# Optimization experiments

Measured on AMD Instinct MI355X. Metric: run time of the kernel, lower is better.

## Reference

```python
import jax, jax.numpy as jnp
import numpy as np

N, STATE_DIM, HID, D_EMB, K = 8192, 512, 128, 128, 10
EPS = 0.001


def setup_inputs() -> dict:
    key = jax.random.key(0)
    ks = jax.random.split(key, 5)
    sc = lambda fan_in: 1.0 / np.sqrt(fan_in)
    return {
        "s": jax.random.normal(ks[0], (N, STATE_DIM), dtype=jnp.float32),
        "W1": jax.random.normal(ks[1], (HID, STATE_DIM), dtype=jnp.float32) * sc(STATE_DIM),
        "b1": jax.random.normal(ks[2], (HID,), dtype=jnp.float32) * sc(STATE_DIM),
        "W2": jax.random.normal(ks[3], (D_EMB, HID), dtype=jnp.float32) * sc(HID),
        "b2": jax.random.normal(ks[4], (D_EMB,), dtype=jnp.float32) * sc(HID),
        "k": K,
    }


def reference(s, W1, b1, W2, b2, k):
    # embedding: relu(Linear) -> Linear
    x = jax.nn.relu(s @ W1.T + b1) @ W2.T + b2            # [N, d_emb]
    # pairwise L2 distance matrix: ||xi||^2 + ||xj||^2 - 2 xi.xj
    sq = jnp.sum(x * x, axis=1)                            # [N]
    dist2 = sq[:, None] + sq[None, :] - 2.0 * (x @ x.T)    # [N, N]
    # clamp tiny negative values from cancellation (torch.sqrt would NaN)
    dist = jnp.sqrt(jnp.maximum(dist2, 1e-12))             # [N, N]
    # k nearest per row, excluding self (smallest entry = own distance ~0)
    neg_vals, _ = jax.lax.top_k(-dist, k + 1)              # [N, k+1], ascending dist
    k_nearest = -neg_vals[:, 1:]                           # [N, k]
    sum_k_nearest = jnp.sum(k_nearest, axis=1, keepdims=True)  # [N, 1]
    mean_k_nearest_2 = jnp.mean(sum_k_nearest) ** 2
    return EPS / (sum_k_nearest ** 2 / mean_k_nearest_2 + EPS)
```

## Files before the change

### kernel.cpp

```cpp
#include <hip/hip_runtime.h>
#include <hip/hip_bf16.h>

#define NN 8192
#define SD 512
#define HID 128
#define DE 128
#define KP1 11
#define EPSF 0.001f
#define NSPLIT 16
#define NCHUNK NSPLIT
#define TILE 64
#define NTILE ((NN / NSPLIT) / TILE)

using short8 = __attribute__((ext_vector_type(8))) short;
using f32x4 = __attribute__((ext_vector_type(4))) float;

__device__ inline ushort f2bf(float f) {
    __hip_bfloat16 b = __float2bfloat16(f);
    return *reinterpret_cast<ushort*>(&b);
}
__device__ inline float bf2f(ushort u) {
    unsigned v = (unsigned)u << 16;
    union { unsigned u; float f; } c; c.u = v; return c.f;
}

__global__ __launch_bounds__(256) void wsplit_kernel(
    const float* __restrict__ W1, const float* __restrict__ W2,
    ushort* __restrict__ W1h, ushort* __restrict__ W1l,
    ushort* __restrict__ W2h, ushort* __restrict__ W2l)
{
    const int bid = blockIdx.x;
    const float* src; ushort *dh, *dl; int base;
    if (bid < 64) { src = W1; dh = W1h; dl = W1l; base = bid * 1024; }
    else          { src = W2; dh = W2h; dl = W2l; base = (bid - 64) * 1024; }
    const int i = base + threadIdx.x * 4;
    float4 f = *reinterpret_cast<const float4*>(src + i);
    ushort h[4], lo[4];
    float fv[4] = {f.x, f.y, f.z, f.w};
#pragma unroll
    for (int j = 0; j < 4; ++j) {
        h[j] = f2bf(fv[j]);
        lo[j] = f2bf(fv[j] - bf2f(h[j]));
    }
    *reinterpret_cast<uint2*>(dh + i) = *reinterpret_cast<uint2*>(h);
    *reinterpret_cast<uint2*>(dl + i) = *reinterpret_cast<uint2*>(lo);
}

__global__ __launch_bounds__(256) void mlp_kernel(
    const float* __restrict__ s, const ushort* __restrict__ W1h,
    const ushort* __restrict__ W1l, const float* __restrict__ b1,
    const ushort* __restrict__ W2h, const ushort* __restrict__ W2l,
    const float* __restrict__ b2, __hip_bfloat16* __restrict__ xb,
    float* __restrict__ sqb)
{
    __shared__ __align__(16) ushort sbh[2][32 * 32];
    __shared__ __align__(16) ushort sbl[2][32 * 32];
    __shared__ __align__(16) ushort hbh[32 * 128];
    __shared__ __align__(16) ushort hbl[32 * 128];
    __shared__ __align__(16) ushort xtile[32 * 128];
    __shared__ float sqpart[4 * 32];

    const int t = threadIdx.x;
    const int w = t >> 6, l = t & 63;
    const int lc = l & 15, c4 = l >> 4;
    const int rb = blockIdx.x * 32;
    const int cb = w * 32;

    const int srow = t >> 3, skq = t & 7;
    const int ssl = ((skq >> 1) + (srow >> 2)) & 3;
    const int sByte = srow * 64 + (ssl ^ (srow & 3)) * 16 + (skq & 1) * 8;
    const float* sgbase = s + (size_t)(rb + srow) * SD + skq * 4;

    float4 sf;
#define STAGE_LOAD_S(kt_) sf = *reinterpret_cast<const float4*>(sgbase + (kt_) * 32)
#define STAGE_WRITE_S(b_) do { \
    float fv_[4] = {sf.x, sf.y, sf.z, sf.w}; \
    ushort h_[4], lo_[4]; \
    _Pragma("unroll") \
    for (int j_ = 0; j_ < 4; ++j_) { \
        h_[j_] = f2bf(fv_[j_]); \
        lo_[j_] = f2bf(fv_[j_] - bf2f(h_[j_])); \
    } \
    *reinterpret_cast<uint2*>(reinterpret_cast<char*>(sbh[b_]) + sByte) = *reinterpret_cast<uint2*>(h_); \
    *reinterpret_cast<uint2*>(reinterpret_cast<char*>(sbl[b_]) + sByte) = *reinterpret_cast<uint2*>(lo_); \
} while (0)

    int aByte[2];
#pragma unroll
    for (int rt = 0; rt < 2; ++rt) {
        int row = rt * 16 + lc;
        int sl = ((c4 + (row >> 2)) & 3) ^ (row & 3);
        aByte[rt] = row * 64 + sl * 16;
    }

    const ushort* w1hp[2]; const ushort* w1lp[2];
#pragma unroll
    for (int ct = 0; ct < 2; ++ct) {
        int col = cb + ct * 16 + lc;
        w1hp[ct] = W1h + (size_t)col * SD + c4 * 8;
        w1lp[ct] = W1l + (size_t)col * SD + c4 * 8;
    }

    f32x4 acc1[2][2];
#pragma unroll
    for (int rt = 0; rt < 2; ++rt)
#pragma unroll
        for (int ct = 0; ct < 2; ++ct) acc1[rt][ct] = {0.f, 0.f, 0.f, 0.f};

    STAGE_LOAD_S(0);
    STAGE_WRITE_S(0);
    short8 bh[2], bl[2], nbh[2], nbl[2];
#pragma unroll
    for (int ct = 0; ct < 2; ++ct) {
        bh[ct] = *reinterpret_cast<const short8*>(w1hp[ct]);
        bl[ct] = *reinterpret_cast<const short8*>(w1lp[ct]);
    }

    for (int kt = 0; kt < 16; ++kt) {
        __syncthreads();
        if (kt < 15) STAGE_LOAD_S(kt + 1);
        short8 ah[2], al[2];
#pragma unroll
        for (int rt = 0; rt < 2; ++rt) {
            ah[rt] = *reinterpret_cast<const short8*>(
                reinterpret_cast<char*>(sbh[kt & 1]) + aByte[rt]);
            al[rt] = *reinterpret_cast<const short8*>(
                reinterpret_cast<char*>(sbl[kt & 1]) + aByte[rt]);
        }
        if (kt < 15) {
#pragma unroll
            for (int ct = 0; ct < 2; ++ct) {
                nbh[ct] = *reinterpret_cast<const short8*>(w1hp[ct] + (kt + 1) * 32);
                nbl[ct] = *reinterpret_cast<const short8*>(w1lp[ct] + (kt + 1) * 32);
            }
        }
#pragma unroll
        for (int rt = 0; rt < 2; ++rt)
#pragma unroll
            for (int ct = 0; ct < 2; ++ct) {
                acc1[rt][ct] = __builtin_amdgcn_mfma_f32_16x16x32_bf16(ah[rt], bh[ct], acc1[rt][ct], 0, 0, 0);
                acc1[rt][ct] = __builtin_amdgcn_mfma_f32_16x16x32_bf16(ah[rt], bl[ct], acc1[rt][ct], 0, 0, 0);
                acc1[rt][ct] = __builtin_amdgcn_mfma_f32_16x16x32_bf16(al[rt], bh[ct], acc1[rt][ct], 0, 0, 0);
            }
        if (kt < 15) {
            STAGE_WRITE_S((kt + 1) & 1);
#pragma unroll
            for (int ct = 0; ct < 2; ++ct) { bh[ct] = nbh[ct]; bl[ct] = nbl[ct]; }
        }
    }

    float b1v[2];
#pragma unroll
    for (int ct = 0; ct < 2; ++ct) b1v[ct] = b1[cb + ct * 16 + lc];
#pragma unroll
    for (int rt = 0; rt < 2; ++rt)
#pragma unroll
        for (int ct = 0; ct < 2; ++ct)
#pragma unroll
            for (int reg = 0; reg < 4; ++reg) {
                float v = fmaxf(acc1[rt][ct][reg] + b1v[ct], 0.f);
                ushort hh = f2bf(v);
                ushort hl = f2bf(v - bf2f(hh));
                int row = rt * 16 + c4 * 4 + reg;
                int kcol = cb + ct * 16 + lc;
                int sl = (kcol >> 3) ^ (row & 15);
                int byte = row * 256 + sl * 16 + (kcol & 7) * 2;
                *reinterpret_cast<ushort*>(reinterpret_cast<char*>(hbh) + byte) = hh;
                *reinterpret_cast<ushort*>(reinterpret_cast<char*>(hbl) + byte) = hl;
            }
    __syncthreads();

    f32x4 acc2[2][2];
#pragma unroll
    for (int rt = 0; rt < 2; ++rt)
#pragma unroll
        for (int ct = 0; ct < 2; ++ct) acc2[rt][ct] = {0.f, 0.f, 0.f, 0.f};

#pragma unroll
    for (int kt = 0; kt < 4; ++kt) {
        short8 ah[2], al[2];
#pragma unroll
        for (int rt = 0; rt < 2; ++rt) {
            int row = rt * 16 + lc;
            int sl = (kt * 4 + c4) ^ (row & 15);
            int byte = row * 256 + sl * 16;
            ah[rt] = *reinterpret_cast<const short8*>(reinterpret_cast<char*>(hbh) + byte);
            al[rt] = *reinterpret_cast<const short8*>(reinterpret_cast<char*>(hbl) + byte);
        }
        short8 wh[2], wl[2];
#pragma unroll
        for (int ct = 0; ct < 2; ++ct) {
            int col = cb + ct * 16 + lc;
            wh[ct] = *reinterpret_cast<const short8*>(W2h + (size_t)col * HID + kt * 32 + c4 * 8);
            wl[ct] = *reinterpret_cast<const short8*>(W2l + (size_t)col * HID + kt * 32 + c4 * 8);
        }
#pragma unroll
        for (int rt = 0; rt < 2; ++rt)
#pragma unroll
            for (int ct = 0; ct < 2; ++ct) {
                acc2[rt][ct] = __builtin_amdgcn_mfma_f32_16x16x32_bf16(ah[rt], wh[ct], acc2[rt][ct], 0, 0, 0);
                acc2[rt][ct] = __builtin_amdgcn_mfma_f32_16x16x32_bf16(ah[rt], wl[ct], acc2[rt][ct], 0, 0, 0);
                acc2[rt][ct] = __builtin_amdgcn_mfma_f32_16x16x32_bf16(al[rt], wh[ct], acc2[rt][ct], 0, 0, 0);
            }
    }

    float b2v[2];
#pragma unroll
    for (int ct = 0; ct < 2; ++ct) b2v[ct] = b2[cb + ct * 16 + lc];
    float p[8];
#pragma unroll
    for (int j = 0; j < 8; ++j) p[j] = 0.f;
#pragma unroll
    for (int rt = 0; rt < 2; ++rt)
#pragma unroll
        for (int ct = 0; ct < 2; ++ct)
#pragma unroll
            for (int reg = 0; reg < 4; ++reg) {
                float v = acc2[rt][ct][reg] + b2v[ct];
                ushort xv = f2bf(v);
                float xf = bf2f(xv);
                p[rt * 4 + reg] = fmaf(xf, xf, p[rt * 4 + reg]);
                int row = rt * 16 + c4 * 4 + reg;
                int e = cb + ct * 16 + lc;
                xtile[row * 128 + e] = xv;
            }
#pragma unroll
    for (int j = 0; j < 8; ++j) {
#pragma unroll
        for (int off = 8; off >= 1; off >>= 1) p[j] += __shfl_xor(p[j], off, 16);
    }
    if (lc == 0) {
#pragma unroll
        for (int rt = 0; rt < 2; ++rt)
#pragma unroll
            for (int reg = 0; reg < 4; ++reg)
                sqpart[w * 32 + rt * 16 + c4 * 4 + reg] = p[rt * 4 + reg];
    }
    __syncthreads();
    if (t < 32)
        sqb[rb + t] = sqpart[t] + sqpart[32 + t] + sqpart[64 + t] + sqpart[96 + t];
    const short8* xsv = reinterpret_cast<const short8*>(xtile);
    short8* xg = reinterpret_cast<short8*>(reinterpret_cast<ushort*>(xb) + (size_t)rb * DE);
    xg[t] = xsv[t];
    xg[t + 256] = xsv[t + 256];
}

__global__ __launch_bounds__(256) void knn_kernel(
    const ushort* __restrict__ xs, const float* __restrict__ sqb,
    float* __restrict__ part)
{
    __shared__ __align__(16) ushort lbuf[2][TILE * DE];
    __shared__ __align__(16) float sqs[NN / NSPLIT];

    const int bid = blockIdx.x;
    const int rid = bid >> 4, cid = bid & 15;
    const int t = threadIdx.x;
    const int w = t >> 6, l = t & 63;
    const int q16 = l & 15, lg = l >> 4;
    const int kk = lg * 8;
    const int qb = rid * 128 + w * 32;
    const int cstart = cid * (NN / NSPLIT);

    short8 bq[2][4];
#pragma unroll
    for (int qs = 0; qs < 2; ++qs)
#pragma unroll
        for (int kb = 0; kb < 4; ++kb)
            bq[qs][kb] = *reinterpret_cast<const short8*>(
                xs + (size_t)(qb + qs * 16 + q16) * DE + kb * 32 + kk);

    float m[2][KP1];
#pragma unroll
    for (int qs = 0; qs < 2; ++qs)
#pragma unroll
        for (int j = 0; j < KP1; ++j) m[qs][j] = 1e30f;

#define INS(qs_, v_) do { \
    float d2_ = (v_); \
    _Pragma("unroll") \
    for (int j_ = KP1 - 1; j_ >= 1; --j_) \
        m[qs_][j_] = __builtin_amdgcn_fmed3f(d2_, m[qs_][j_ - 1], m[qs_][j_]); \
    m[qs_][0] = fminf(d2_, m[qs_][0]); \
} while (0)

    if (t < 128)
        reinterpret_cast<float4*>(sqs)[t] =
            reinterpret_cast<const float4*>(sqb + cstart)[t];

    int gIdx[4], dIdx[4];
#pragma unroll
    for (int i = 0; i < 4; ++i) {
        int sl = t + 256 * i;
        int row = sl >> 4, col = sl & 15;
        gIdx[i] = row * DE + col * 8;
        dIdx[i] = (row * 16 + (col ^ (row & 7))) * 8;
    }
    int aIdx[4];
#pragma unroll
    for (int kb = 0; kb < 4; ++kb)
        aIdx[kb] = (q16 * 16 + ((kb * 4 + lg) ^ (q16 & 7))) * 8;

    short8 st[4];
#define STAGE_LOAD(tt_) do { \
    const ushort* sb_ = xs + (size_t)(cstart + (tt_) * TILE) * DE; \
    _Pragma("unroll") \
    for (int i_ = 0; i_ < 4; ++i_) \
        st[i_] = *reinterpret_cast<const short8*>(sb_ + gIdx[i_]); \
} while (0)
#define STAGE_WRITE(nb_) do { \
    _Pragma("unroll") \
    for (int i_ = 0; i_ < 4; ++i_) \
        *reinterpret_cast<short8*>(&lbuf[nb_][dIdx[i_]]) = st[i_]; \
} while (0)

    STAGE_LOAD(0);
    STAGE_WRITE(0);

    for (int tt = 0; tt < NTILE; ++tt) {
        __syncthreads();
        if (tt + 1 < NTILE) STAGE_LOAD(tt + 1);
        const ushort* lb = lbuf[tt & 1];
#pragma unroll
        for (int cs = 0; cs < 4; ++cs) {
            short8 fa[4];
#pragma unroll
            for (int kb = 0; kb < 4; ++kb)
                fa[kb] = *reinterpret_cast<const short8*>(lb + cs * 2048 + aIdx[kb]);
            float4 sv = *reinterpret_cast<const float4*>(sqs + tt * TILE + cs * 16 + lg * 4);
#pragma unroll
            for (int qs = 0; qs < 2; ++qs) {
                f32x4 acc = {0.f, 0.f, 0.f, 0.f};
#pragma unroll
                for (int kb = 0; kb < 4; ++kb)
                    acc = __builtin_amdgcn_mfma_f32_16x16x32_bf16(fa[kb], bq[qs][kb], acc, 0, 0, 0);
                INS(qs, fmaf(-2.f, acc[0], sv.x));
                INS(qs, fmaf(-2.f, acc[1], sv.y));
                INS(qs, fmaf(-2.f, acc[2], sv.z));
                INS(qs, fmaf(-2.f, acc[3], sv.w));
            }
        }
        if (tt + 1 < NTILE) STAGE_WRITE((tt + 1) & 1);
    }
#undef STAGE_LOAD
#undef STAGE_WRITE
#undef INS

    __syncthreads();
    float* mb = reinterpret_cast<float*>(lbuf);
#pragma unroll
    for (int qs = 0; qs < 2; ++qs)
#pragma unroll
        for (int j = 0; j < KP1; ++j)
            mb[(((w * 2 + qs) * 4 + lg) * KP1 + j) * 16 + q16] = m[qs][j];
    __syncthreads();
    if (l < 32) {
        const int qs = l >> 4, qq = l & 15;
        float mm[KP1];
#pragma unroll
        for (int j = 0; j < KP1; ++j)
            mm[j] = mb[(((w * 2 + qs) * 4 + 0) * KP1 + j) * 16 + qq];
#pragma unroll
        for (int g = 1; g < 4; ++g)
#pragma unroll
            for (int j = 0; j < KP1; ++j) {
                float d2 = mb[(((w * 2 + qs) * 4 + g) * KP1 + j) * 16 + qq];
#pragma unroll
                for (int jj = KP1 - 1; jj >= 1; --jj)
                    mm[jj] = __builtin_amdgcn_fmed3f(d2, mm[jj - 1], mm[jj]);
                mm[0] = fminf(d2, mm[0]);
            }
        const int q = qb + qs * 16 + qq;
#pragma unroll
        for (int j = 0; j < KP1; ++j)
            part[(size_t)(cid * KP1 + j) * NN + q] = mm[j];
    }
}

__global__ __launch_bounds__(256) void merge_kernel(
    const float* __restrict__ part, const float* __restrict__ sqb,
    float* __restrict__ sumk, float* __restrict__ psum)
{
    const int row = blockIdx.x * 256 + threadIdx.x;
    float m[KP1];
#pragma unroll
    for (int j = 0; j < KP1; ++j) m[j] = 1e30f;
#pragma unroll
    for (int ch = 0; ch < NCHUNK; ++ch) {
#pragma unroll
        for (int j = 0; j < KP1; ++j) {
            float d2 = part[(size_t)(ch * KP1 + j) * NN + row];
#pragma unroll
            for (int jj = KP1 - 1; jj >= 1; --jj)
                m[jj] = __builtin_amdgcn_fmed3f(d2, m[jj - 1], m[jj]);
            m[0] = fminf(d2, m[0]);
        }
    }
    const float sqq = sqb[row];
    float sum = 0.f;
#pragma unroll
    for (int j = 1; j < KP1; ++j)
        sum += sqrtf(fmaxf(m[j] + sqq, 1e-12f));
    sumk[row] = sum;

    float p = sum;
#pragma unroll
    for (int off = 32; off >= 1; off >>= 1) p += __shfl_xor(p, off, 64);
    __shared__ float red[4];
    if ((threadIdx.x & 63) == 0) red[threadIdx.x >> 6] = p;
    __syncthreads();
    if (threadIdx.x == 0) psum[blockIdx.x] = red[0] + red[1] + red[2] + red[3];
}

__global__ void reduce_kernel(const float* __restrict__ psum, float* __restrict__ qv)
{
    const int t = threadIdx.x;
    float p = (t < 32) ? psum[t] : 0.f;
#pragma unroll
    for (int off = 32; off >= 1; off >>= 1) p += __shfl_xor(p, off, 64);
    if (t == 0) {
        float mean = p * (1.0f / NN);
        qv[0] = EPSF * mean * mean;
    }
}

__global__ __launch_bounds__(256) void final_kernel(
    const float* __restrict__ sumk, const float* __restrict__ qv,
    float* __restrict__ out)
{
    const int i = blockIdx.x * 256 + threadIdx.x;
    const float qq = qv[0];
    const float sv = sumk[i];
    out[i] = qq / (fmaf(sv, sv, qq));
}

extern "C" void kernel_launch(void* const* d_in, const int* in_sizes, int n_in,
                              void* d_out, int out_size, void* d_ws, size_t ws_size,
                              hipStream_t stream)
{
    const float* s  = (const float*)d_in[0];
    const float* W1 = (const float*)d_in[1];
    const float* b1 = (const float*)d_in[2];
    const float* W2 = (const float*)d_in[3];
    const float* b2 = (const float*)d_in[4];
    float* out = (float*)d_out;

    char* ws = (char*)d_ws;
    __hip_bfloat16* xb = (__hip_bfloat16*)ws;
    float* sqb  = (float*)(ws + (size_t)NN * DE * 2);
    float* part = sqb + NN;
    float* sumk = part + (size_t)NCHUNK * KP1 * NN;
    float* psum = sumk + NN;
    float* qv   = psum + 32;
    ushort* W1h = (ushort*)(qv + 1);
    ushort* W1l = W1h + (size_t)HID * SD;
    ushort* W2h = W1l + (size_t)HID * SD;
    ushort* W2l = W2h + (size_t)DE * HID;

    wsplit_kernel<<<80, 256, 0, stream>>>(W1, W2, W1h, W1l, W2h, W2l);
    mlp_kernel<<<NN / 32, 256, 0, stream>>>(s, W1h, W1l, b1, W2h, W2l, b2, xb, sqb);
    knn_kernel<<<(NN / 128) * NSPLIT, 256, 0, stream>>>((const ushort*)xb, sqb, part);
    merge_kernel<<<NN / 256, 256, 0, stream>>>(part, sqb, sumk, psum);
    reduce_kernel<<<1, 64, 0, stream>>>(psum, qv);
    final_kernel<<<NN / 256, 256, 0, stream>>>(sumk, qv, out);
}
```

Measured before the change: 79.53 us.

## Pre-scale candidates by -2, fold norms into MFMA accumulator, double KNN column splits

The MLP kernel now also writes a bf16 copy of the embeddings scaled by -2. The KNN kernel streams that copy as candidates and seeds the MFMA accumulator with the squared norms, which removes the per-element fma before insertion. Column splits double to 32 with 32-row tiles, launch bounds request 6 waves per SIMD, and the final per-block merge is done one query half at a time to cut LDS use. This adds parallelism and occupancy but doubles the partial-results traffic seen by the merge kernel, adds an extra embedding write, and rounds -2x to bf16.

```diff
diff --git a/kernel.cpp b/kernel.cpp
--- a/kernel.cpp
+++ b/kernel.cpp
@@ -7,9 +7,9 @@
 #define DE 128
 #define KP1 11
 #define EPSF 0.001f
-#define NSPLIT 16
+#define NSPLIT 32
 #define NCHUNK NSPLIT
-#define TILE 64
+#define TILE 32
 #define NTILE ((NN / NSPLIT) / TILE)
 
 using short8 = __attribute__((ext_vector_type(8))) short;
@@ -51,13 +51,14 @@
     const ushort* __restrict__ W1l, const float* __restrict__ b1,
     const ushort* __restrict__ W2h, const ushort* __restrict__ W2l,
     const float* __restrict__ b2, __hip_bfloat16* __restrict__ xb,
-    float* __restrict__ sqb)
+    __hip_bfloat16* __restrict__ xb2, float* __restrict__ sqb)
 {
     __shared__ __align__(16) ushort sbh[2][32 * 32];
     __shared__ __align__(16) ushort sbl[2][32 * 32];
     __shared__ __align__(16) ushort hbh[32 * 128];
     __shared__ __align__(16) ushort hbl[32 * 128];
     __shared__ __align__(16) ushort xtile[32 * 128];
+    __shared__ __align__(16) ushort xtile2[32 * 128];
     __shared__ float sqpart[4 * 32];
 
     const int t = threadIdx.x;
@@ -223,6 +224,7 @@
                 int row = rt * 16 + c4 * 4 + reg;
                 int e = cb + ct * 16 + lc;
                 xtile[row * 128 + e] = xv;
+                xtile2[row * 128 + e] = f2bf(-2.f * xf);
             }
 #pragma unroll
     for (int j = 0; j < 8; ++j) {
@@ -243,17 +245,21 @@
     short8* xg = reinterpret_cast<short8*>(reinterpret_cast<ushort*>(xb) + (size_t)rb * DE);
     xg[t] = xsv[t];
     xg[t + 256] = xsv[t + 256];
-}
-
-__global__ __launch_bounds__(256) void knn_kernel(
-    const ushort* __restrict__ xs, const float* __restrict__ sqb,
-    float* __restrict__ part)
+    const short8* xsv2 = reinterpret_cast<const short8*>(xtile2);
+    short8* xg2 = reinterpret_cast<short8*>(reinterpret_cast<ushort*>(xb2) + (size_t)rb * DE);
+    xg2[t] = xsv2[t];
+    xg2[t + 256] = xsv2[t + 256];
+}
+
+__global__ __launch_bounds__(256, 6) void knn_kernel(
+    const ushort* __restrict__ xs, const ushort* __restrict__ xs2,
+    const float* __restrict__ sqb, float* __restrict__ part)
 {
     __shared__ __align__(16) ushort lbuf[2][TILE * DE];
     __shared__ __align__(16) float sqs[NN / NSPLIT];
 
     const int bid = blockIdx.x;
-    const int rid = bid >> 4, cid = bid & 15;
+    const int rid = bid >> 5, cid = bid & 31;
     const int t = threadIdx.x;
     const int w = t >> 6, l = t & 63;
     const int q16 = l & 15, lg = l >> 4;
@@ -283,13 +289,13 @@
     m[qs_][0] = fminf(d2_, m[qs_][0]); \
 } while (0)
 
-    if (t < 128)
+    if (t < 64)
         reinterpret_cast<float4*>(sqs)[t] =
             reinterpret_cast<const float4*>(sqb + cstart)[t];
 
-    int gIdx[4], dIdx[4];
-#pragma unroll
-    for (int i = 0; i < 4; ++i) {
+    int gIdx[2], dIdx[2];
+#pragma unroll
+    for (int i = 0; i < 2; ++i) {
         int sl = t + 256 * i;
         int row = sl >> 4, col = sl & 15;
         gIdx[i] = row * DE + col * 8;
@@ -300,17 +306,15 @@
     for (int kb = 0; kb < 4; ++kb)
         aIdx[kb] = (q16 * 16 + ((kb * 4 + lg) ^ (q16 & 7))) * 8;
 
-    short8 st[4];
+    short8 st[2];
 #define STAGE_LOAD(tt_) do { \
-    const ushort* sb_ = xs + (size_t)(cstart + (tt_) * TILE) * DE; \
-    _Pragma("unroll") \
-    for (int i_ = 0; i_ < 4; ++i_) \
-        st[i_] = *reinterpret_cast<const short8*>(sb_ + gIdx[i_]); \
+    const ushort* sb_ = xs2 + (size_t)(cstart + (tt_) * TILE) * DE; \
+    st[0] = *reinterpret_cast<const short8*>(sb_ + gIdx[0]); \
+    st[1] = *reinterpret_cast<const short8*>(sb_ + gIdx[1]); \
 } while (0)
 #define STAGE_WRITE(nb_) do { \
-    _Pragma("unroll") \
-    for (int i_ = 0; i_ < 4; ++i_) \
-        *reinterpret_cast<short8*>(&lbuf[nb_][dIdx[i_]]) = st[i_]; \
+    *reinterpret_cast<short8*>(&lbuf[nb_][dIdx[0]]) = st[0]; \
+    *reinterpret_cast<short8*>(&lbuf[nb_][dIdx[1]]) = st[1]; \
 } while (0)
 
     STAGE_LOAD(0);
@@ -321,7 +325,7 @@
         if (tt + 1 < NTILE) STAGE_LOAD(tt + 1);
         const ushort* lb = lbuf[tt & 1];
 #pragma unroll
-        for (int cs = 0; cs < 4; ++cs) {
+        for (int cs = 0; cs < 2; ++cs) {
             short8 fa[4];
 #pragma unroll
             for (int kb = 0; kb < 4; ++kb)
@@ -329,14 +333,14 @@
             float4 sv = *reinterpret_cast<const float4*>(sqs + tt * TILE + cs * 16 + lg * 4);
 #pragma unroll
             for (int qs = 0; qs < 2; ++qs) {
-                f32x4 acc = {0.f, 0.f, 0.f, 0.f};
+                f32x4 acc = {sv.x, sv.y, sv.z, sv.w};
 #pragma unroll
                 for (int kb = 0; kb < 4; ++kb)
                     acc = __builtin_amdgcn_mfma_f32_16x16x32_bf16(fa[kb], bq[qs][kb], acc, 0, 0, 0);
-                INS(qs, fmaf(-2.f, acc[0], sv.x));
-                INS(qs, fmaf(-2.f, acc[1], sv.y));
-                INS(qs, fmaf(-2.f, acc[2], sv.z));
-                INS(qs, fmaf(-2.f, acc[3], sv.w));
+                INS(qs, acc[0]);
+                INS(qs, acc[1]);
+                INS(qs, acc[2]);
+                INS(qs, acc[3]);
             }
         }
         if (tt + 1 < NTILE) STAGE_WRITE((tt + 1) & 1);
@@ -345,34 +349,34 @@
 #undef STAGE_WRITE
 #undef INS
 
-    __syncthreads();
     float* mb = reinterpret_cast<float*>(lbuf);
 #pragma unroll
-    for (int qs = 0; qs < 2; ++qs)
+    for (int qs = 0; qs < 2; ++qs) {
+        __syncthreads();
 #pragma unroll
         for (int j = 0; j < KP1; ++j)
-            mb[(((w * 2 + qs) * 4 + lg) * KP1 + j) * 16 + q16] = m[qs][j];
-    __syncthreads();
-    if (l < 32) {
-        const int qs = l >> 4, qq = l & 15;
-        float mm[KP1];
-#pragma unroll
-        for (int j = 0; j < KP1; ++j)
-            mm[j] = mb[(((w * 2 + qs) * 4 + 0) * KP1 + j) * 16 + qq];
-#pragma unroll
-        for (int g = 1; g < 4; ++g)
-#pragma unroll
-            for (int j = 0; j < KP1; ++j) {
-                float d2 = mb[(((w * 2 + qs) * 4 + g) * KP1 + j) * 16 + qq];
-#pragma unroll
-                for (int jj = KP1 - 1; jj >= 1; --jj)
-                    mm[jj] = __builtin_amdgcn_fmed3f(d2, mm[jj - 1], mm[jj]);
-                mm[0] = fminf(d2, mm[0]);
-            }
-        const int q = qb + qs * 16 + qq;
-#pragma unroll
-        for (int j = 0; j < KP1; ++j)
-            part[(size_t)(cid * KP1 + j) * NN + q] = mm[j];
+            mb[((w * 4 + lg) * KP1 + j) * 16 + q16] = m[qs][j];
+        __syncthreads();
+        if (l < 16) {
+            float mm[KP1];
+#pragma unroll
+            for (int j = 0; j < KP1; ++j)
+                mm[j] = mb[((w * 4 + 0) * KP1 + j) * 16 + l];
+#pragma unroll
+            for (int g = 1; g < 4; ++g)
+#pragma unroll
+                for (int j = 0; j < KP1; ++j) {
+                    float d2 = mb[((w * 4 + g) * KP1 + j) * 16 + l];
+#pragma unroll
+                    for (int jj = KP1 - 1; jj >= 1; --jj)
+                        mm[jj] = __builtin_amdgcn_fmed3f(d2, mm[jj - 1], mm[jj]);
+                    mm[0] = fminf(d2, mm[0]);
+                }
+            const int q = qb + qs * 16 + l;
+#pragma unroll
+            for (int j = 0; j < KP1; ++j)
+                part[(size_t)(cid * KP1 + j) * NN + q] = mm[j];
+        }
     }
 }
 
@@ -384,7 +388,7 @@
     float m[KP1];
 #pragma unroll
     for (int j = 0; j < KP1; ++j) m[j] = 1e30f;
-#pragma unroll
+#pragma unroll 4
     for (int ch = 0; ch < NCHUNK; ++ch) {
 #pragma unroll
         for (int j = 0; j < KP1; ++j) {
@@ -445,8 +449,9 @@
     float* out = (float*)d_out;
 
     char* ws = (char*)d_ws;
-    __hip_bfloat16* xb = (__hip_bfloat16*)ws;
-    float* sqb  = (float*)(ws + (size_t)NN * DE * 2);
+    __hip_bfloat16* xb  = (__hip_bfloat16*)ws;
+    __hip_bfloat16* xb2 = xb + (size_t)NN * DE;
+    float* sqb  = (float*)(ws + (size_t)2 * NN * DE * 2);
     float* part = sqb + NN;
     float* sumk = part + (size_t)NCHUNK * KP1 * NN;
     float* psum = sumk + NN;
@@ -457,8 +462,9 @@
     ushort* W2l = W2h + (size_t)DE * HID;
 
     wsplit_kernel<<<80, 256, 0, stream>>>(W1, W2, W1h, W1l, W2h, W2l);
-    mlp_kernel<<<NN / 32, 256, 0, stream>>>(s, W1h, W1l, b1, W2h, W2l, b2, xb, sqb);
-    knn_kernel<<<(NN / 128) * NSPLIT, 256, 0, stream>>>((const ushort*)xb, sqb, part);
+    mlp_kernel<<<NN / 32, 256, 0, stream>>>(s, W1h, W1l, b1, W2h, W2l, b2, xb, xb2, sqb);
+    knn_kernel<<<(NN / 128) * NSPLIT, 256, 0, stream>>>(
+        (const ushort*)xb, (const ushort*)xb2, sqb, part);
     merge_kernel<<<NN / 256, 256, 0, stream>>>(part, sqb, sumk, psum);
     reduce_kernel<<<1, 64, 0, stream>>>(psum, qv);
     final_kernel<<<NN / 256, 256, 0, stream>>>(sumk, qv, out);
```

Measured after the change: 111.6 us. 1.4x slower.

## Load whole column block into LDS once, widen knn blocks, fuse reduce into final

Applied to the files above, without the earlier changes.

The knn kernel now uses 512-thread blocks covering 256 query rows and 32 column splits. Each block loads its entire 256-row column chunk of embeddings into LDS once, replacing the double-buffered 64-row tile pipeline and its per-tile barriers. Partial top-k results are written in a per-block contiguous layout, and merge reads them back with matching indexing over 32 chunks. The single-block reduce kernel is folded into the final kernel, which removes one launch at the cost of every block redundantly summing the 32 partial sums. In exchange, the merge reads twice as many partial lists, and the larger per-block LDS footprint may limit occupancy.

```diff
diff --git a/kernel.cpp b/kernel.cpp
--- a/kernel.cpp
+++ b/kernel.cpp
@@ -7,10 +7,11 @@
 #define DE 128
 #define KP1 11
 #define EPSF 0.001f
-#define NSPLIT 16
+#define NSPLIT 32
 #define NCHUNK NSPLIT
-#define TILE 64
-#define NTILE ((NN / NSPLIT) / TILE)
+#define CB (NN / NSPLIT)
+#define NSUB (CB / 16)
+#define PBLK (8 * 2 * KP1 * 16)
 
 using short8 = __attribute__((ext_vector_type(8))) short;
 using f32x4 = __attribute__((ext_vector_type(4))) float;
@@ -245,21 +246,35 @@
     xg[t + 256] = xsv[t + 256];
 }
 
-__global__ __launch_bounds__(256) void knn_kernel(
+__global__ __launch_bounds__(512) void knn_kernel(
     const ushort* __restrict__ xs, const float* __restrict__ sqb,
     float* __restrict__ part)
 {
-    __shared__ __align__(16) ushort lbuf[2][TILE * DE];
-    __shared__ __align__(16) float sqs[NN / NSPLIT];
+    __shared__ __align__(16) ushort lbuf[CB * DE];
+    __shared__ __align__(16) float sqs[CB];
 
     const int bid = blockIdx.x;
-    const int rid = bid >> 4, cid = bid & 15;
+    const int rid = bid >> 5, cid = bid & 31;
     const int t = threadIdx.x;
     const int w = t >> 6, l = t & 63;
     const int q16 = l & 15, lg = l >> 4;
     const int kk = lg * 8;
-    const int qb = rid * 128 + w * 32;
-    const int cstart = cid * (NN / NSPLIT);
+    const int qb = rid * 256 + w * 32;
+    const int cstart = cid * CB;
+
+    {
+        const ushort* sb = xs + (size_t)cstart * DE;
+#pragma unroll
+        for (int i = 0; i < 8; ++i) {
+            int sl = t + 512 * i;
+            int row = sl >> 4, col = sl & 15;
+            short8 v = *reinterpret_cast<const short8*>(sb + row * DE + col * 8);
+            *reinterpret_cast<short8*>(&lbuf[(row * 16 + (col ^ (row & 7))) * 8]) = v;
+        }
+        if (t < 64)
+            reinterpret_cast<float4*>(sqs)[t] =
+                reinterpret_cast<const float4*>(sqb + cstart)[t];
+    }
 
     short8 bq[2][4];
 #pragma unroll
@@ -283,67 +298,32 @@
     m[qs_][0] = fminf(d2_, m[qs_][0]); \
 } while (0)
 
-    if (t < 128)
-        reinterpret_cast<float4*>(sqs)[t] =
-            reinterpret_cast<const float4*>(sqb + cstart)[t];
-
-    int gIdx[4], dIdx[4];
-#pragma unroll
-    for (int i = 0; i < 4; ++i) {
-        int sl = t + 256 * i;
-        int row = sl >> 4, col = sl & 15;
-        gIdx[i] = row * DE + col * 8;
-        dIdx[i] = (row * 16 + (col ^ (row & 7))) * 8;
-    }
     int aIdx[4];
 #pragma unroll
     for (int kb = 0; kb < 4; ++kb)
         aIdx[kb] = (q16 * 16 + ((kb * 4 + lg) ^ (q16 & 7))) * 8;
 
-    short8 st[4];
-#define STAGE_LOAD(tt_) do { \
-    const ushort* sb_ = xs + (size_t)(cstart + (tt_) * TILE) * DE; \
-    _Pragma("unroll") \
-    for (int i_ = 0; i_ < 4; ++i_) \
-        st[i_] = *reinterpret_cast<const short8*>(sb_ + gIdx[i_]); \
-} while (0)
-#define STAGE_WRITE(nb_) do { \
-    _Pragma("unroll") \
-    for (int i_ = 0; i_ < 4; ++i_) \
-        *reinterpret_cast<short8*>(&lbuf[nb_][dIdx[i_]]) = st[i_]; \
-} while (0)
-
-    STAGE_LOAD(0);
-    STAGE_WRITE(0);
-
-    for (int tt = 0; tt < NTILE; ++tt) {
-        __syncthreads();
-        if (tt + 1 < NTILE) STAGE_LOAD(tt + 1);
-        const ushort* lb = lbuf[tt & 1];
-#pragma unroll
-        for (int cs = 0; cs < 4; ++cs) {
-            short8 fa[4];
+    __syncthreads();
+
+    for (int st = 0; st < NSUB; ++st) {
+        const ushort* lb = lbuf + st * 2048;
+        short8 fa[4];
+#pragma unroll
+        for (int kb = 0; kb < 4; ++kb)
+            fa[kb] = *reinterpret_cast<const short8*>(lb + aIdx[kb]);
+        float4 sv = *reinterpret_cast<const float4*>(sqs + st * 16 + lg * 4);
+#pragma unroll
+        for (int qs = 0; qs < 2; ++qs) {
+            f32x4 acc = {0.f, 0.f, 0.f, 0.f};
 #pragma unroll
             for (int kb = 0; kb < 4; ++kb)
-                fa[kb] = *reinterpret_cast<const short8*>(lb + cs * 2048 + aIdx[kb]);
-            float4 sv = *reinterpret_cast<const float4*>(sqs + tt * TILE + cs * 16 + lg * 4);
-#pragma unroll
-            for (int qs = 0; qs < 2; ++qs) {
-                f32x4 acc = {0.f, 0.f, 0.f, 0.f};
-#pragma unroll
-                for (int kb = 0; kb < 4; ++kb)
-                    acc = __builtin_amdgcn_mfma_f32_16x16x32_bf16(fa[kb], bq[qs][kb], acc, 0, 0, 0);
-                INS(qs, fmaf(-2.f, acc[0], sv.x));
-                INS(qs, fmaf(-2.f, acc[1], sv.y));
-                INS(qs, fmaf(-2.f, acc[2], sv.z));
-                INS(qs, fmaf(-2.f, acc[3], sv.w));
-            }
-        }
-        if (tt + 1 < NTILE) STAGE_WRITE((tt + 1) & 1);
-    }
-#undef STAGE_LOAD
-#undef STAGE_WRITE
-#undef INS
+                acc = __builtin_amdgcn_mfma_f32_16x16x32_bf16(fa[kb], bq[qs][kb], acc, 0, 0, 0);
+            INS(qs, fmaf(-2.f, acc[0], sv.x));
+            INS(qs, fmaf(-2.f, acc[1], sv.y));
+            INS(qs, fmaf(-2.f, acc[2], sv.z));
+            INS(qs, fmaf(-2.f, acc[3], sv.w));
+        }
+    }
 
     __syncthreads();
     float* mb = reinterpret_cast<float*>(lbuf);
@@ -369,10 +349,10 @@
                     mm[jj] = __builtin_amdgcn_fmed3f(d2, mm[jj - 1], mm[jj]);
                 mm[0] = fminf(d2, mm[0]);
             }
-        const int q = qb + qs * 16 + qq;
+        float* pout = part + (size_t)bid * PBLK;
 #pragma unroll
         for (int j = 0; j < KP1; ++j)
-            part[(size_t)(cid * KP1 + j) * NN + q] = mm[j];
+            pout[((w * 2 + qs) * KP1 + j) * 16 + qq] = mm[j];
     }
 }
 
@@ -381,14 +361,20 @@
     float* __restrict__ sumk, float* __restrict__ psum)
 {
     const int row = blockIdx.x * 256 + threadIdx.x;
+    const int rid = row >> 8;
+    const int sub = ((row >> 5) & 7) * 2 + ((row >> 4) & 1);
+    const int lane = row & 15;
+    const float* pbase = part + (size_t)rid * NSPLIT * PBLK + sub * (KP1 * 16) + lane;
+
     float m[KP1];
 #pragma unroll
     for (int j = 0; j < KP1; ++j) m[j] = 1e30f;
-#pragma unroll
+#pragma unroll 4
     for (int ch = 0; ch < NCHUNK; ++ch) {
+        const float* pc = pbase + ch * PBLK;
 #pragma unroll
         for (int j = 0; j < KP1; ++j) {
-            float d2 = part[(size_t)(ch * KP1 + j) * NN + row];
+            float d2 = pc[j * 16];
 #pragma unroll
             for (int jj = KP1 - 1; jj >= 1; --jj)
                 m[jj] = __builtin_amdgcn_fmed3f(d2, m[jj - 1], m[jj]);
@@ -411,24 +397,24 @@
     if (threadIdx.x == 0) psum[blockIdx.x] = red[0] + red[1] + red[2] + red[3];
 }
 
-__global__ void reduce_kernel(const float* __restrict__ psum, float* __restrict__ qv)
-{
+__global__ __launch_bounds__(256) void final_kernel(
+    const float* __restrict__ sumk, const float* __restrict__ psum,
+    float* __restrict__ out)
+{
+    __shared__ float qsh;
     const int t = threadIdx.x;
-    float p = (t < 32) ? psum[t] : 0.f;
-#pragma unroll
-    for (int off = 32; off >= 1; off >>= 1) p += __shfl_xor(p, off, 64);
-    if (t == 0) {
-        float mean = p * (1.0f / NN);
-        qv[0] = EPSF * mean * mean;
-    }
-}
-
-__global__ __launch_bounds__(256) void final_kernel(
-    const float* __restrict__ sumk, const float* __restrict__ qv,
-    float* __restrict__ out)
-{
-    const int i = blockIdx.x * 256 + threadIdx.x;
-    const float qq = qv[0];
+    if (t < 64) {
+        float p = (t < 32) ? psum[t] : 0.f;
+#pragma unroll
+        for (int off = 32; off >= 1; off >>= 1) p += __shfl_xor(p, off, 64);
+        if (t == 0) {
+            float mean = p * (1.0f / NN);
+            qsh = EPSF * mean * mean;
+        }
+    }
+    __syncthreads();
+    const float qq = qsh;
+    const int i = blockIdx.x * 256 + t;
     const float sv = sumk[i];
     out[i] = qq / (fmaf(sv, sv, qq));
 }
@@ -448,18 +434,16 @@
     __hip_bfloat16* xb = (__hip_bfloat16*)ws;
     float* sqb  = (float*)(ws + (size_t)NN * DE * 2);
     float* part = sqb + NN;
-    float* sumk = part + (size_t)NCHUNK * KP1 * NN;
+    float* sumk = part + (size_t)1024 * PBLK;
     float* psum = sumk + NN;
-    float* qv   = psum + 32;
-    ushort* W1h = (ushort*)(qv + 1);
+    ushort* W1h = (ushort*)(psum + 32);
     ushort* W1l = W1h + (size_t)HID * SD;
     ushort* W2h = W1l + (size_t)HID * SD;
     ushort* W2l = W2h + (size_t)DE * HID;
 
     wsplit_kernel<<<80, 256, 0, stream>>>(W1, W2, W1h, W1l, W2h, W2l);
     mlp_kernel<<<NN / 32, 256, 0, stream>>>(s, W1h, W1l, b1, W2h, W2l, b2, xb, sqb);
-    knn_kernel<<<(NN / 128) * NSPLIT, 256, 0, stream>>>((const ushort*)xb, sqb, part);
+    knn_kernel<<<(NN / 256) * NSPLIT, 512, 0, stream>>>((const ushort*)xb, sqb, part);
     merge_kernel<<<NN / 256, 256, 0, stream>>>(part, sqb, sumk, psum);
-    reduce_kernel<<<1, 64, 0, stream>>>(psum, qv);
-    final_kernel<<<NN / 256, 256, 0, stream>>>(sumk, qv, out);
-}
+    final_kernel<<<NN / 256, 256, 0, stream>>>(sumk, psum, out);
+}
```

Result: no change. 80.01 us (+0.6%).
